# Optimization experiments

Hardware: AMD Instinct MI355X
Metric: run time of the kernel (lower is better)

Reference implementation:

```python
import jax, jax.numpy as jnp
import numpy as np

B, S, D, H = 2, 2048, 2048, 16
HD = D // H  # head dim = 128

def setup_inputs() -> dict:
    key = jax.random.key(0)
    ks = jax.random.split(key, 5)
    x = jax.random.normal(ks[0], (B, S, D), dtype=jnp.float32)
    # causal mask: True means block that position (per docstring)
    mask = jnp.triu(jnp.ones((S, S), dtype=bool), k=1)
    scale = 1.0 / np.sqrt(D)
    Wq = jax.random.normal(ks[1], (D, D), dtype=jnp.float32) * scale
    Wk = jax.random.normal(ks[2], (D, D), dtype=jnp.float32) * scale
    Wv = jax.random.normal(ks[3], (D, D), dtype=jnp.float32) * scale
    Wo = jax.random.normal(ks[4], (D, D), dtype=jnp.float32) * scale
    return {"x": x, "mask": mask, "Wq": Wq, "Wk": Wk, "Wv": Wv, "Wo": Wo}

def _split_heads(t):
    b, s, _ = t.shape
    return t.reshape(b, s, H, HD).transpose(0, 2, 1, 3)  # (b, h, s, hd)

def reference(x, mask, Wq, Wk, Wv, Wo):
    # nn.Linear(bias=False): y = x @ W.T
    q = _split_heads(x @ Wq.T)
    k = _split_heads(x @ Wk.T)
    v = _split_heads(x @ Wv.T)
    scale = HD ** -0.5
    scores = jnp.einsum('bhqd,bhkd->bhqk', q, k) * scale  # (b,h,s,s)
    scores = jnp.where(mask[None, None, :, :], -jnp.inf, scores)
    weights = jax.nn.softmax(scores, axis=-1)  # dropout is identity at eval
    out = jnp.einsum('bhqk,bhkd->bhqd', weights, v)
    out = out.transpose(0, 2, 1, 3).reshape(x.shape[0], x.shape[1], D)
    return out @ Wo.T
```

## Files before the change

kernel.cpp:

```cpp
#include <hip/hip_runtime.h>
#include <hip/hip_bf16.h>

typedef __bf16 bf16x8 __attribute__((ext_vector_type(8)));
typedef float f32x4 __attribute__((ext_vector_type(4)));
typedef unsigned short ushort8v __attribute__((ext_vector_type(8)));

__device__ __forceinline__ unsigned short f2bf(float f) {
    unsigned int u = __float_as_uint(f);
    u = (u + 0x7fffu + ((u >> 16) & 1u)) >> 16;
    return (unsigned short)u;
}

__device__ __forceinline__ f32x4 mfma16(bf16x8 a, bf16x8 b, f32x4 c) {
    return __builtin_amdgcn_mfma_f32_16x16x32_bf16(a, b, c, 0, 0, 0);
}

__device__ __forceinline__ void store_c(unsigned short* p, float v) { *p = f2bf(v); }
__device__ __forceinline__ void store_c(float* p, float v) { *p = v; }

__global__ __launch_bounds__(256) void cast_f32_bf16(const float* __restrict__ in,
                                                     unsigned short* __restrict__ out,
                                                     int n4) {
    int i = blockIdx.x * blockDim.x + threadIdx.x;
    if (i < n4) {
        float4 f = ((const float4*)in)[i];
        ushort4 u;
        u.x = f2bf(f.x); u.y = f2bf(f.y); u.z = f2bf(f.z); u.w = f2bf(f.w);
        ((ushort4*)out)[i] = u;
    }
}

__global__ __launch_bounds__(256) void transpose_v(const unsigned short* __restrict__ v,
                                                   unsigned short* __restrict__ vt) {
    __shared__ unsigned short t[64][65];
    const int tid = threadIdx.x;
    const int s0 = blockIdx.x * 64;
    const int d0 = blockIdx.y * 64;
    const int bh = blockIdx.z;
    const int b = bh >> 4, h = bh & 15;

#pragma unroll
    for (int i = 0; i < 2; ++i) {
        int idx = i * 256 + tid;
        int r = idx >> 3, c8 = (idx & 7) * 8;
        ushort8v d = *(const ushort8v*)(v + ((size_t)(b * 2048 + s0 + r)) * 2048 + h * 128 + d0 + c8);
#pragma unroll
        for (int j = 0; j < 8; ++j) t[r][c8 + j] = d[j];
    }
    __syncthreads();
#pragma unroll
    for (int i = 0; i < 2; ++i) {
        int idx = i * 256 + tid;
        int dr = idx >> 3, sc8 = (idx & 7) * 8;
        ushort8v o;
#pragma unroll
        for (int j = 0; j < 8; ++j) o[j] = t[sc8 + j][dr];
        *(ushort8v*)(vt + ((size_t)(bh * 128 + d0 + dr)) * 2048 + s0 + sc8) = o;
    }
}

__device__ __forceinline__ void stage3(const unsigned short* __restrict__ A,
                                       const unsigned short* __restrict__ B,
                                       char* lAslot, char* lBslot,
                                       int row0, int col0, int kt, int K,
                                       int tid, int w) {
#pragma unroll
    for (int j = 0; j < 4; ++j) {
        int ci = j * 512 + tid;
        int r = ci >> 3, p = ci & 7;
        int c = p ^ (r & 7);
        size_t goff = ((size_t)(row0 + r) * K + kt + c * 8) * 2;
        __builtin_amdgcn_global_load_lds(
            (__attribute__((address_space(1))) void*)(void*)((const char*)A + goff),
            (__attribute__((address_space(3))) void*)(lAslot + (j * 512 + w * 64) * 16),
            16, 0, 0);
    }
#pragma unroll
    for (int j = 0; j < 2; ++j) {
        int ci = j * 512 + tid;
        int r = ci >> 3, p = ci & 7;
        int c = p ^ (r & 7);
        size_t goff = ((size_t)(col0 + r) * K + kt + c * 8) * 2;
        __builtin_amdgcn_global_load_lds(
            (__attribute__((address_space(1))) void*)(void*)((const char*)B + goff),
            (__attribute__((address_space(3))) void*)(lBslot + (j * 512 + w * 64) * 16),
            16, 0, 0);
    }
}

template <typename OUT_T>
__global__ __launch_bounds__(512) void gemm_bt3(const unsigned short* __restrict__ A,
                                                const unsigned short* __restrict__ B,
                                                OUT_T* __restrict__ C,
                                                int M, int N, int K) {
    __shared__ __align__(16) unsigned short lA[3][256 * 64];
    __shared__ __align__(16) unsigned short lB[3][128 * 64];

    const int tid = threadIdx.x;
    const int w = tid >> 6, lane = tid & 63;
    const int wm = w >> 1, wn = w & 1;
    const int lane16 = lane & 15, g = lane >> 4;
    const int row0 = blockIdx.y * 256, col0 = blockIdx.x * 128;
    const int NT = K >> 6;

    f32x4 acc[4][4] = {};

    stage3(A, B, (char*)lA[0], (char*)lB[0], row0, col0, 0,   K, tid, w);
    stage3(A, B, (char*)lA[1], (char*)lB[1], row0, col0, 64,  K, tid, w);
    stage3(A, B, (char*)lA[2], (char*)lB[2], row0, col0, 128, K, tid, w);

    int s = 0;
#pragma unroll 1
    for (int t = 0; t < NT; ++t) {
        if (t + 2 < NT)      asm volatile("s_waitcnt vmcnt(12)" ::: "memory");
        else if (t + 1 < NT) asm volatile("s_waitcnt vmcnt(6)" ::: "memory");
        else                 asm volatile("s_waitcnt vmcnt(0)" ::: "memory");
        __builtin_amdgcn_s_barrier();
        asm volatile("" ::: "memory");

#pragma unroll
        for (int kk = 0; kk < 2; ++kk) {
            bf16x8 aF[4], bF[4];
#pragma unroll
            for (int f = 0; f < 4; ++f) {
                int r = wm * 64 + f * 16 + lane16;
                aF[f] = *(const bf16x8*)&lA[s][r * 64 + ((kk * 4 + g) ^ (r & 7)) * 8];
            }
#pragma unroll
            for (int f = 0; f < 4; ++f) {
                int r = wn * 64 + f * 16 + lane16;
                bF[f] = *(const bf16x8*)&lB[s][r * 64 + ((kk * 4 + g) ^ (r & 7)) * 8];
            }
            __builtin_amdgcn_s_setprio(1);
#pragma unroll
            for (int mf = 0; mf < 4; ++mf)
#pragma unroll
                for (int nf = 0; nf < 4; ++nf)
                    acc[mf][nf] = mfma16(aF[mf], bF[nf], acc[mf][nf]);
            __builtin_amdgcn_s_setprio(0);
        }

        asm volatile("" ::: "memory");
        __builtin_amdgcn_s_barrier();
        asm volatile("" ::: "memory");

        if (t + 3 < NT)
            stage3(A, B, (char*)lA[s], (char*)lB[s], row0, col0, (t + 3) * 64, K, tid, w);
        s = (s == 2) ? 0 : s + 1;
    }

#pragma unroll
    for (int mf = 0; mf < 4; ++mf) {
        int r0 = row0 + wm * 64 + mf * 16 + g * 4;
#pragma unroll
        for (int nf = 0; nf < 4; ++nf) {
            int c = col0 + wn * 64 + nf * 16 + lane16;
#pragma unroll
            for (int r = 0; r < 4; ++r)
                store_c(&C[(size_t)(r0 + r) * N + c], acc[mf][nf][r]);
        }
    }
}

__global__ __launch_bounds__(256) void attn_causal(const unsigned short* __restrict__ Q,
                                                   const unsigned short* __restrict__ K,
                                                   const unsigned short* __restrict__ VT,
                                                   unsigned short* __restrict__ O) {
    __shared__ __align__(16) unsigned short lK[64 * 128];
    __shared__ __align__(16) unsigned short lVt[128 * 64];
    __shared__ __align__(16) unsigned short lP[4][16 * 80];

    const int tid = threadIdx.x, w = tid >> 6, lane = tid & 63;
    const int lane16 = lane & 15, g = lane >> 4;
    const int bh = blockIdx.y;
    const int b = bh >> 4, h = bh & 15;
    const size_t rowBase = (size_t)b * 2048;
    const int hoff = h * 128;
    const float scale = 0.08838834764831845f;

    for (int pass = 0; pass < 2; ++pass) {
        const int qt = pass ? (31 - (int)blockIdx.x) : (int)blockIdx.x;
        const int qt0 = qt * 64;
        const int qr0 = qt0 + w * 16;

        bf16x8 qa[4];
        {
            const unsigned short* qp = Q + (rowBase + qr0 + lane16) * 2048 + hoff;
#pragma unroll
            for (int kk = 0; kk < 4; ++kk)
                qa[kk] = *(const bf16x8*)(qp + kk * 32 + g * 8);
        }

        float m_r[4], l_r[4];
        f32x4 accO[8];
#pragma unroll
        for (int r = 0; r < 4; ++r) { m_r[r] = -1e30f; l_r[r] = 0.f; }
#pragma unroll
        for (int f = 0; f < 8; ++f) accO[f] = f32x4{0.f, 0.f, 0.f, 0.f};

        const int nt = qt + 1;

        for (int t = 0; t < nt; ++t) {
            const int kv0 = t * 64;
            __syncthreads();
#pragma unroll
            for (int i = 0; i < 4; ++i) {
                int ci = (w * 4 + i) * 64 + lane;
                int krow = ci >> 4;
                int kcolb = ((ci & 15) ^ (krow & 7)) * 16;
                size_t goff = ((rowBase + kv0 + krow) * 2048 + hoff) * 2 + kcolb;
                __builtin_amdgcn_global_load_lds(
                    (__attribute__((address_space(1))) void*)(void*)((const char*)K + goff),
                    (__attribute__((address_space(3))) void*)((char*)lK + (w * 4 + i) * 1024),
                    16, 0, 0);
            }
#pragma unroll
            for (int i = 0; i < 4; ++i) {
                int ci = (w * 4 + i) * 64 + lane;
                int drow = ci >> 3;
                int slot = (ci & 7) ^ (drow & 7);
                size_t goff = ((size_t)(bh * 128 + drow) * 2048 + kv0 + slot * 8) * 2;
                __builtin_amdgcn_global_load_lds(
                    (__attribute__((address_space(1))) void*)(void*)((const char*)VT + goff),
                    (__attribute__((address_space(3))) void*)((char*)lVt + (w * 4 + i) * 1024),
                    16, 0, 0);
            }
            __syncthreads();

            float p[4][4];
#pragma unroll
            for (int n = 0; n < 4; ++n) {
                f32x4 sc = {0.f, 0.f, 0.f, 0.f};
                int row = n * 16 + lane16;
#pragma unroll
                for (int kk = 0; kk < 4; ++kk) {
                    int sw = (kk * 4 + g) ^ (row & 7);
                    bf16x8 kb = *(const bf16x8*)&lK[row * 128 + sw * 8];
                    sc = mfma16(qa[kk], kb, sc);
                }
#pragma unroll
                for (int r = 0; r < 4; ++r) p[n][r] = sc[r] * scale;
            }
            if (t == nt - 1) {
#pragma unroll
                for (int n = 0; n < 4; ++n)
#pragma unroll
                    for (int r = 0; r < 4; ++r) {
                        int qi = qr0 + g * 4 + r, ki = kv0 + n * 16 + lane16;
                        if (ki > qi) p[n][r] = -1e30f;
                    }
            }
#pragma unroll
            for (int r = 0; r < 4; ++r) {
                float rm = fmaxf(fmaxf(p[0][r], p[1][r]), fmaxf(p[2][r], p[3][r]));
#pragma unroll
                for (int off = 1; off < 16; off <<= 1)
                    rm = fmaxf(rm, __shfl_xor(rm, off, 64));
                float mn = fmaxf(m_r[r], rm);
                float fac = __expf(m_r[r] - mn);
                float rs = 0.f;
#pragma unroll
                for (int n = 0; n < 4; ++n) { p[n][r] = __expf(p[n][r] - mn); rs += p[n][r]; }
#pragma unroll
                for (int off = 1; off < 16; off <<= 1)
                    rs += __shfl_xor(rs, off, 64);
                l_r[r] = l_r[r] * fac + rs;
                m_r[r] = mn;
#pragma unroll
                for (int f = 0; f < 8; ++f) accO[f][r] *= fac;
            }
#pragma unroll
            for (int n = 0; n < 4; ++n)
#pragma unroll
                for (int r = 0; r < 4; ++r)
                    lP[w][(g * 4 + r) * 80 + n * 16 + lane16] = f2bf(p[n][r]);
            asm volatile("s_waitcnt lgkmcnt(0)" ::: "memory");
#pragma unroll
            for (int kk2 = 0; kk2 < 2; ++kk2) {
                bf16x8 pa = *(const bf16x8*)&lP[w][lane16 * 80 + kk2 * 32 + g * 8];
#pragma unroll
                for (int f = 0; f < 8; ++f) {
                    int row = f * 16 + lane16;
                    int slot = (kk2 * 4 + g) ^ (row & 7);
                    bf16x8 vb = *(const bf16x8*)&lVt[row * 64 + slot * 8];
                    accO[f] = mfma16(pa, vb, accO[f]);
                }
            }
        }

#pragma unroll
        for (int f = 0; f < 8; ++f)
#pragma unroll
            for (int r = 0; r < 4; ++r) {
                float ov = accO[f][r] / l_r[r];
                O[(rowBase + qr0 + g * 4 + r) * 2048 + hoff + f * 16 + lane16] = f2bf(ov);
            }
    }
}

extern "C" void kernel_launch(void* const* d_in, const int* in_sizes, int n_in,
                              void* d_out, int out_size, void* d_ws, size_t ws_size,
                              hipStream_t stream) {
    const float* x  = (const float*)d_in[0];
    const float* Wq = (const float*)d_in[2];
    const float* Wk = (const float*)d_in[3];
    const float* Wv = (const float*)d_in[4];
    const float* Wo = (const float*)d_in[5];
    float* out = (float*)d_out;

    char* ws = (char*)d_ws;
    unsigned short* xb = (unsigned short*)(ws);
    unsigned short* q  = (unsigned short*)(ws + (size_t)(16u << 20));
    unsigned short* k  = (unsigned short*)(ws + (size_t)(32u << 20));
    unsigned short* v  = (unsigned short*)(ws + (size_t)(48u << 20));
    unsigned short* wb = (unsigned short*)(ws + (size_t)(64u << 20));
    unsigned short* vt = xb;
    unsigned short* o  = v;

    const int M = 4096, D = 2048;
    dim3 gg(D / 128, M / 256);

    cast_f32_bf16<<<(M * D / 4) / 256, 256, 0, stream>>>(x, xb, M * D / 4);

    cast_f32_bf16<<<(D * D / 4) / 256, 256, 0, stream>>>(Wq, wb, D * D / 4);
    gemm_bt3<unsigned short><<<gg, 512, 0, stream>>>(xb, wb, q, M, D, D);
    cast_f32_bf16<<<(D * D / 4) / 256, 256, 0, stream>>>(Wk, wb, D * D / 4);
    gemm_bt3<unsigned short><<<gg, 512, 0, stream>>>(xb, wb, k, M, D, D);
    cast_f32_bf16<<<(D * D / 4) / 256, 256, 0, stream>>>(Wv, wb, D * D / 4);
    gemm_bt3<unsigned short><<<gg, 512, 0, stream>>>(xb, wb, v, M, D, D);

    transpose_v<<<dim3(32, 2, 32), 256, 0, stream>>>(v, vt);

    attn_causal<<<dim3(16, 32), 256, 0, stream>>>(q, k, vt, o);

    cast_f32_bf16<<<(D * D / 4) / 256, 256, 0, stream>>>(Wo, wb, D * D / 4);
    gemm_bt3<float><<<gg, 512, 0, stream>>>(o, wb, out, M, D, D);
}
```

Baseline: 445.6 us.

## Fuse Q/K projections into one 256x256-tile GEMM and widen attention query tiles

```diff
diff --git a/kernel.cpp b/kernel.cpp
--- a/kernel.cpp
+++ b/kernel.cpp
@@ -162,13 +162,117 @@
     }
 }
 
-__global__ __launch_bounds__(256) void attn_causal(const unsigned short* __restrict__ Q,
+__device__ __forceinline__ void stage4(const unsigned short* __restrict__ A,
+                                       const unsigned short* __restrict__ B,
+                                       char* lAslot, char* lBslot,
+                                       int row0, int bcol0, int kt, int K,
+                                       int tid, int w) {
+#pragma unroll
+    for (int j = 0; j < 4; ++j) {
+        int ci = j * 512 + tid;
+        int r = ci >> 3, p = ci & 7;
+        int c = p ^ (r & 7);
+        size_t goff = ((size_t)(row0 + r) * K + kt + c * 8) * 2;
+        __builtin_amdgcn_global_load_lds(
+            (__attribute__((address_space(1))) void*)(void*)((const char*)A + goff),
+            (__attribute__((address_space(3))) void*)(lAslot + (j * 512 + w * 64) * 16),
+            16, 0, 0);
+    }
+#pragma unroll
+    for (int j = 0; j < 4; ++j) {
+        int ci = j * 512 + tid;
+        int r = ci >> 3, p = ci & 7;
+        int c = p ^ (r & 7);
+        size_t goff = ((size_t)(bcol0 + r) * K + kt + c * 8) * 2;
+        __builtin_amdgcn_global_load_lds(
+            (__attribute__((address_space(1))) void*)(void*)((const char*)B + goff),
+            (__attribute__((address_space(3))) void*)(lBslot + (j * 512 + w * 64) * 16),
+            16, 0, 0);
+    }
+}
+
+__global__ __launch_bounds__(512) void gemm_qk(const unsigned short* __restrict__ A,
+                                               const unsigned short* __restrict__ B,
+                                               unsigned short* __restrict__ Cq,
+                                               unsigned short* __restrict__ Ck,
+                                               int M, int K) {
+    __shared__ __align__(16) unsigned short lA[2][256 * 64];
+    __shared__ __align__(16) unsigned short lB[2][256 * 64];
+
+    const int tid = threadIdx.x;
+    const int w = tid >> 6, lane = tid & 63;
+    const int wm = w >> 2, wn = w & 3;
+    const int lane16 = lane & 15, g = lane >> 4;
+    const int bx = blockIdx.x;
+    const int row0 = blockIdx.y * 256;
+    const int bcol0 = bx * 256;
+    unsigned short* Cout = (bx < 8) ? Cq : Ck;
+    const int col0 = bcol0 & 2047;
+    const int NT = K >> 6;
+
+    f32x4 acc[8][4] = {};
+
+    stage4(A, B, (char*)lA[0], (char*)lB[0], row0, bcol0, 0,  K, tid, w);
+    stage4(A, B, (char*)lA[1], (char*)lB[1], row0, bcol0, 64, K, tid, w);
+
+#pragma unroll 1
+    for (int t = 0; t < NT; ++t) {
+        const int s = t & 1;
+        if (t + 1 < NT) asm volatile("s_waitcnt vmcnt(8)" ::: "memory");
+        else            asm volatile("s_waitcnt vmcnt(0)" ::: "memory");
+        __builtin_amdgcn_s_barrier();
+        asm volatile("" ::: "memory");
+
+#pragma unroll
+        for (int kk = 0; kk < 2; ++kk) {
+            bf16x8 aF[8], bF[4];
+#pragma unroll
+            for (int f = 0; f < 8; ++f) {
+                int r = wm * 128 + f * 16 + lane16;
+                aF[f] = *(const bf16x8*)&lA[s][r * 64 + ((kk * 4 + g) ^ (r & 7)) * 8];
+            }
+#pragma unroll
+            for (int f = 0; f < 4; ++f) {
+                int r = wn * 64 + f * 16 + lane16;
+                bF[f] = *(const bf16x8*)&lB[s][r * 64 + ((kk * 4 + g) ^ (r & 7)) * 8];
+            }
+            __builtin_amdgcn_s_setprio(1);
+#pragma unroll
+            for (int mf = 0; mf < 8; ++mf)
+#pragma unroll
+                for (int nf = 0; nf < 4; ++nf)
+                    acc[mf][nf] = mfma16(aF[mf], bF[nf], acc[mf][nf]);
+            __builtin_amdgcn_s_setprio(0);
+        }
+
+        asm volatile("" ::: "memory");
+        __builtin_amdgcn_s_barrier();
+        asm volatile("" ::: "memory");
+
+        if (t + 2 < NT)
+            stage4(A, B, (char*)lA[s], (char*)lB[s], row0, bcol0, (t + 2) * 64, K, tid, w);
+    }
+
+#pragma unroll
+    for (int mf = 0; mf < 8; ++mf) {
+        int r0 = row0 + wm * 128 + mf * 16 + g * 4;
+#pragma unroll
+        for (int nf = 0; nf < 4; ++nf) {
+            int c = col0 + wn * 64 + nf * 16 + lane16;
+#pragma unroll
+            for (int r = 0; r < 4; ++r)
+                store_c(&Cout[(size_t)(r0 + r) * 2048 + c], acc[mf][nf][r]);
+        }
+    }
+}
+
+__global__ __launch_bounds__(512) void attn_causal(const unsigned short* __restrict__ Q,
                                                    const unsigned short* __restrict__ K,
                                                    const unsigned short* __restrict__ VT,
                                                    unsigned short* __restrict__ O) {
     __shared__ __align__(16) unsigned short lK[64 * 128];
     __shared__ __align__(16) unsigned short lVt[128 * 64];
-    __shared__ __align__(16) unsigned short lP[4][16 * 80];
+    __shared__ __align__(16) unsigned short lP[8][16 * 80];
 
     const int tid = threadIdx.x, w = tid >> 6, lane = tid & 63;
     const int lane16 = lane & 15, g = lane >> 4;
@@ -179,8 +283,8 @@
     const float scale = 0.08838834764831845f;
 
     for (int pass = 0; pass < 2; ++pass) {
-        const int qt = pass ? (31 - (int)blockIdx.x) : (int)blockIdx.x;
-        const int qt0 = qt * 64;
+        const int qt = pass ? (15 - (int)blockIdx.x) : (int)blockIdx.x;
+        const int qt0 = qt * 128;
         const int qr0 = qt0 + w * 16;
 
         bf16x8 qa[4];
@@ -198,31 +302,31 @@
 #pragma unroll
         for (int f = 0; f < 8; ++f) accO[f] = f32x4{0.f, 0.f, 0.f, 0.f};
 
-        const int nt = qt + 1;
+        const int nt = 2 * (qt + 1);
 
         for (int t = 0; t < nt; ++t) {
             const int kv0 = t * 64;
             __syncthreads();
 #pragma unroll
-            for (int i = 0; i < 4; ++i) {
-                int ci = (w * 4 + i) * 64 + lane;
+            for (int i = 0; i < 2; ++i) {
+                int ci = i * 512 + w * 64 + lane;
                 int krow = ci >> 4;
                 int kcolb = ((ci & 15) ^ (krow & 7)) * 16;
                 size_t goff = ((rowBase + kv0 + krow) * 2048 + hoff) * 2 + kcolb;
                 __builtin_amdgcn_global_load_lds(
                     (__attribute__((address_space(1))) void*)(void*)((const char*)K + goff),
-                    (__attribute__((address_space(3))) void*)((char*)lK + (w * 4 + i) * 1024),
+                    (__attribute__((address_space(3))) void*)((char*)lK + (i * 512 + w * 64) * 16),
                     16, 0, 0);
             }
 #pragma unroll
-            for (int i = 0; i < 4; ++i) {
-                int ci = (w * 4 + i) * 64 + lane;
+            for (int i = 0; i < 2; ++i) {
+                int ci = i * 512 + w * 64 + lane;
                 int drow = ci >> 3;
                 int slot = (ci & 7) ^ (drow & 7);
                 size_t goff = ((size_t)(bh * 128 + drow) * 2048 + kv0 + slot * 8) * 2;
                 __builtin_amdgcn_global_load_lds(
                     (__attribute__((address_space(1))) void*)(void*)((const char*)VT + goff),
-                    (__attribute__((address_space(3))) void*)((char*)lVt + (w * 4 + i) * 1024),
+                    (__attribute__((address_space(3))) void*)((char*)lVt + (i * 512 + w * 64) * 16),
                     16, 0, 0);
             }
             __syncthreads();
@@ -241,7 +345,7 @@
 #pragma unroll
                 for (int r = 0; r < 4; ++r) p[n][r] = sc[r] * scale;
             }
-            if (t == nt - 1) {
+            if (t >= nt - 2) {
 #pragma unroll
                 for (int n = 0; n < 4; ++n)
 #pragma unroll
@@ -309,30 +413,30 @@
     float* out = (float*)d_out;
 
     char* ws = (char*)d_ws;
-    unsigned short* xb = (unsigned short*)(ws);
-    unsigned short* q  = (unsigned short*)(ws + (size_t)(16u << 20));
-    unsigned short* k  = (unsigned short*)(ws + (size_t)(32u << 20));
-    unsigned short* v  = (unsigned short*)(ws + (size_t)(48u << 20));
-    unsigned short* wb = (unsigned short*)(ws + (size_t)(64u << 20));
-    unsigned short* vt = xb;
-    unsigned short* o  = v;
+    unsigned short* xb  = (unsigned short*)(ws);
+    unsigned short* q   = (unsigned short*)(ws + (size_t)(16u << 20));
+    unsigned short* k   = (unsigned short*)(ws + (size_t)(32u << 20));
+    unsigned short* wqk = (unsigned short*)(ws + (size_t)(48u << 20));
+    unsigned short* wb  = (unsigned short*)(ws + (size_t)(64u << 20));
+    unsigned short* v   = wqk;
+    unsigned short* vt  = xb;
+    unsigned short* o   = v;
 
     const int M = 4096, D = 2048;
-    dim3 gg(D / 128, M / 256);
 
     cast_f32_bf16<<<(M * D / 4) / 256, 256, 0, stream>>>(x, xb, M * D / 4);
 
-    cast_f32_bf16<<<(D * D / 4) / 256, 256, 0, stream>>>(Wq, wb, D * D / 4);
-    gemm_bt3<unsigned short><<<gg, 512, 0, stream>>>(xb, wb, q, M, D, D);
-    cast_f32_bf16<<<(D * D / 4) / 256, 256, 0, stream>>>(Wk, wb, D * D / 4);
-    gemm_bt3<unsigned short><<<gg, 512, 0, stream>>>(xb, wb, k, M, D, D);
+    cast_f32_bf16<<<(D * D / 4) / 256, 256, 0, stream>>>(Wq, wqk, D * D / 4);
+    cast_f32_bf16<<<(D * D / 4) / 256, 256, 0, stream>>>(Wk, wqk + (size_t)D * D, D * D / 4);
+    gemm_qk<<<dim3(16, 16), 512, 0, stream>>>(xb, wqk, q, k, M, D);
+
     cast_f32_bf16<<<(D * D / 4) / 256, 256, 0, stream>>>(Wv, wb, D * D / 4);
-    gemm_bt3<unsigned short><<<gg, 512, 0, stream>>>(xb, wb, v, M, D, D);
+    gemm_bt3<unsigned short><<<dim3(16, 16), 512, 0, stream>>>(xb, wb, v, M, D, D);
 
     transpose_v<<<dim3(32, 2, 32), 256, 0, stream>>>(v, vt);
 
-    attn_causal<<<dim3(16, 32), 256, 0, stream>>>(q, k, vt, o);
+    attn_causal<<<dim3(8, 32), 512, 0, stream>>>(q, k, vt, o);
 
     cast_f32_bf16<<<(D * D / 4) / 256, 256, 0, stream>>>(Wo, wb, D * D / 4);
-    gemm_bt3<float><<<gg, 512, 0, stream>>>(o, wb, out, M, D, D);
-}
+    gemm_bt3<float><<<dim3(16, 16), 512, 0, stream>>>(o, wb, out, M, D, D);
+}
```

Result: faster. 431.4 us (-3.2%).
